# Kernel optimization log

Hardware: AMD Instinct MI355X
Metric: run time of the kernel (lower is better)

## Reference

```python
import jax, jax.numpy as jnp
import numpy as np

NUM_EMBEDDINGS = 2048
EMBEDDING_DIM = 512
INPUT_DIM = 256  # input_chan**2 = 16**2
COMMITMENT_COST = 0.25
BN_EPS = 1e-5


def setup_inputs() -> dict:
    key = jax.random.key(0)
    ks = jax.random.split(key, 8)
    B, N = 64, 1024
    inputs = jax.random.normal(ks[0], (B, N, INPUT_DIM), dtype=jnp.float32)
    # embedding init: uniform(-1/K, 1/K) as in the torch module
    emb_scale = 1.0 / NUM_EMBEDDINGS
    embedding = jax.random.uniform(ks[1], (NUM_EMBEDDINGS, EMBEDDING_DIM), dtype=jnp.float32,
                                   minval=-emb_scale, maxval=emb_scale)
    # Linear layers use torch convention W[out, in]
    W1 = jax.random.normal(ks[2], (EMBEDDING_DIM, INPUT_DIM), dtype=jnp.float32) / np.sqrt(INPUT_DIM)
    b1 = jnp.zeros((EMBEDDING_DIM,), dtype=jnp.float32)
    W2 = jax.random.normal(ks[3], (INPUT_DIM, EMBEDDING_DIM), dtype=jnp.float32) / np.sqrt(EMBEDDING_DIM)
    b2 = jnp.zeros((INPUT_DIM,), dtype=jnp.float32)
    # BatchNorm affine params initialized to 1/0 as in the module
    bn1_gamma = jnp.ones((INPUT_DIM,), dtype=jnp.float32)
    bn1_beta = jnp.zeros((INPUT_DIM,), dtype=jnp.float32)
    bn2_gamma = jnp.ones((EMBEDDING_DIM,), dtype=jnp.float32)
    bn2_beta = jnp.zeros((EMBEDDING_DIM,), dtype=jnp.float32)
    return {"inputs": inputs, "bn1_gamma": bn1_gamma, "bn1_beta": bn1_beta,
            "W1": W1, "b1": b1, "embedding": embedding,
            "bn2_gamma": bn2_gamma, "bn2_beta": bn2_beta, "W2": W2, "b2": b2}


def reference(inputs, bn1_gamma, bn1_beta, W1, b1, embedding, bn2_gamma, bn2_beta, W2, b2):
    sg = jax.lax.stop_gradient
    input_shape = inputs.shape
    flat = inputs.reshape(-1, INPUT_DIM)  # [T, D_in]
    # BatchNorm1d in eval mode (running_mean=0, running_var=1); Dropout is identity in eval.
    bn1_scale = 1.0 / jnp.sqrt(1.0 + BN_EPS)
    x = flat * (bn1_gamma * bn1_scale) + bn1_beta
    x = x @ W1.T + b1  # [T, E]
    # pairwise squared distances to codebook, argmin
    distances = (jnp.sum(x * x, axis=1, keepdims=True)
                 + jnp.sum(embedding * embedding, axis=1)
                 - 2.0 * x @ embedding.T)  # [T, K]
    encoding_indices = jnp.argmin(distances, axis=1)  # [T]
    # gather == one-hot @ embedding (same math, same gradient scatter-add)
    quantized = jnp.take(embedding, encoding_indices, axis=0)  # [T, E]
    bn2_scale = 1.0 / jnp.sqrt(1.0 + BN_EPS)
    quantized = quantized * (bn2_gamma * bn2_scale) + bn2_beta
    quantized = (quantized @ W2.T + b2).reshape(input_shape)
    e_latent_loss = jnp.mean((sg(quantized) - inputs) ** 2)
    q_latent_loss = jnp.mean((quantized - sg(inputs)) ** 2)
    loss = q_latent_loss + COMMITMENT_COST * e_latent_loss
    quantized_st = inputs + sg(quantized - inputs)  # straight-through
    T = flat.shape[0]
    usage = jnp.zeros((NUM_EMBEDDINGS,), dtype=jnp.float32).at[encoding_indices].add(1.0) / T
    return (loss, quantized_st, usage)
```

## Files before the change

kernel.cpp:

```cpp
#include <hip/hip_runtime.h>
#include <math.h>
#include <stdint.h>

#define TOK 65536
#define DIN 256
#define EDIM 512
#define KCB 2048
#define NTB 128

#define OFF_MP   0u
#define OFF_CP   524288u
#define OFF_Q    526336u
#define OFF_W2T  1050624u
#define OFF_U    1181696u
#define OFF_CQ   1182208u
#define OFF_BH   1182464u
#define TOT_F    1444608u

typedef short short8 __attribute__((ext_vector_type(8)));
typedef float f32x4 __attribute__((ext_vector_type(4)));

__device__ __forceinline__ unsigned short bf16rne(float x) {
    uint32_t u = __float_as_uint(x);
    u += 0x7fffu + ((u >> 16) & 1u);
    return (unsigned short)(u >> 16);
}
__device__ __forceinline__ void async_load16(const void* g, void* l) {
    __builtin_amdgcn_global_load_lds((const __attribute__((address_space(1))) void*)g,
                                     (__attribute__((address_space(3))) void*)l, 16, 0, 0);
}

__global__ void prep1_kernel(const float* __restrict__ W1, const float* __restrict__ W2,
                             const float* __restrict__ bn1_beta, const float* __restrict__ bn2_gamma,
                             const float* __restrict__ bn2_beta, const float* __restrict__ b2,
                             float* __restrict__ W2T, float* __restrict__ u, float* __restrict__ cQ,
                             float* __restrict__ out) {
    __shared__ float red[256];
    const int b = blockIdx.x, t = threadIdx.x;
    const int gid = b * 256 + t;
    if (gid == 0) out[0] = 0.0f;
    if (gid < KCB) out[1 + TOK * DIN + gid] = 0.0f;
    const float s = 1.0f / sqrtf(1.0f + 1e-5f);
    if (b < EDIM) {
        int e = b;
        W2T[e * DIN + t] = bn2_gamma[e] * s * W2[t * EDIM + e];
        float v = bn1_beta[t] * W1[e * DIN + t];
        red[t] = v; __syncthreads();
        for (int off = 128; off; off >>= 1) { if (t < off) red[t] += red[t + off]; __syncthreads(); }
        if (t == 0) u[e] = red[0];
    } else {
        int o = b - EDIM;
        float v = bn2_beta[t] * W2[o * EDIM + t] + bn2_beta[t + 256] * W2[o * EDIM + t + 256];
        red[t] = v; __syncthreads();
        for (int off = 128; off; off >>= 1) { if (t < off) red[t] += red[t + off]; __syncthreads(); }
        if (t == 0) cQ[o] = b2[o] + red[0];
    }
}

__global__ __launch_bounds__(512) void prep2_kernel(const float* __restrict__ E, const float* __restrict__ W1,
                                                    const float* __restrict__ W2T, const float* __restrict__ bn1_gamma,
                                                    const float* __restrict__ cQ, const float* __restrict__ b1,
                                                    const float* __restrict__ u,
                                                    float* __restrict__ Q, float* __restrict__ cp,
                                                    unsigned short* __restrict__ Bh) {
    __shared__ __align__(16) unsigned short hs[8][264];
    const int t = threadIdx.x;
    const int col = t & 255;
    const int half = __builtin_amdgcn_readfirstlane(t >> 8);
    const int k0 = blockIdx.x * 8;
    const float* __restrict__ Ek = E + ((size_t)k0 + (size_t)half * 4) * EDIM;

    float m[4] = {0, 0, 0, 0};
    float q[4] = {0, 0, 0, 0};
    for (int e0 = 0; e0 < EDIM; e0 += 8) {
        float w1v[8], w2v[8];
#pragma unroll
        for (int j = 0; j < 8; j++) {
            w1v[j] = W1[(e0 + j) * DIN + col];
            w2v[j] = W2T[(e0 + j) * DIN + col];
        }
#pragma unroll
        for (int r = 0; r < 4; r++) {
#pragma unroll
            for (int j = 0; j < 8; j++) {
                float ev = Ek[(size_t)r * EDIM + e0 + j];
                m[r] += ev * w1v[j];
                q[r] += ev * w2v[j];
            }
        }
    }
    const float s = 1.0f / sqrtf(1.0f + 1e-5f);
    const float gs = bn1_gamma[col] * s;
    const float cq = cQ[col];
#pragma unroll
    for (int r = 0; r < 4; r++) {
        Q[(size_t)(k0 + half * 4 + r) * DIN + col] = q[r] + cq;
        hs[half * 4 + r][col] = bf16rne(gs * m[r]);
    }

    {
        const int wv = t >> 6, l = t & 63;
        const float* __restrict__ Er = E + (size_t)(k0 + wv) * EDIM;
        float sa = 0.0f, sb = 0.0f;
#pragma unroll
        for (int i = 0; i < 8; i++) {
            int e = l + i * 64;
            float ev = Er[e];
            float be = b1[e] + u[e];
            sa += ev * be; sb += ev * ev;
        }
        float v = sa - 0.5f * sb;
#pragma unroll
        for (int off = 32; off; off >>= 1) v += __shfl_down(v, off, 64);
        if (l == 0) cp[k0 + wv] = v;
    }

    __syncthreads();

    if (t < 256) {
        const int rr = t & 7, qr = (t >> 3) & 3, kc = t >> 5;
        const int nt = k0 >> 4;
        const int l2 = (k0 & 8) + rr + (qr << 4);
        short8 vh = *(const short8*)&hs[rr][kc * 32 + qr * 8];
        *(short8*)&Bh[((size_t)kc * NTB + nt) * 512 + (size_t)l2 * 8] = vh;
    }
}

__global__ __launch_bounds__(256) void score_fused_kernel(const float* __restrict__ flat,
                                                          const unsigned short* __restrict__ Bh,
                                                          const float* __restrict__ cp,
                                                          const float* __restrict__ Q,
                                                          float* __restrict__ out) {
    __shared__ __align__(16) unsigned short Blds[2][32 * 512];
    __shared__ int ksel[128];
    const int t = threadIdx.x, lane = t & 63, w = t >> 6;
    const int m0 = blockIdx.x * 128;
    const int fr = lane & 15, qr = lane >> 4;

    short8 af[8][2];
#pragma unroll
    for (int kc = 0; kc < 8; kc++)
#pragma unroll
        for (int mt = 0; mt < 2; mt++) {
            int row = m0 + w * 32 + mt * 16 + fr;
            const float* p = flat + (size_t)row * DIN + kc * 32 + qr * 8;
            float4 a = *(const float4*)p;
            float4 b = *(const float4*)(p + 4);
            float f[8] = {a.x, a.y, a.z, a.w, b.x, b.y, b.z, b.w};
            unsigned short* hp = (unsigned short*)&af[kc][mt];
#pragma unroll
            for (int j = 0; j < 8; j++) hp[j] = bf16rne(f[j]);
        }

#pragma unroll
    for (int i = 0; i < 8; i++) {
        int tl = i * 4 + w;
        int kc = tl >> 2, nt = tl & 3;
        async_load16(Bh + ((size_t)kc * NTB + nt) * 512 + lane * 8,
                     &Blds[0][tl * 512 + lane * 8]);
    }
    __syncthreads();

    float bestv[2][4];
    int besti[2][4];
#pragma unroll
    for (int mt = 0; mt < 2; mt++)
#pragma unroll
        for (int r = 0; r < 4; r++) { bestv[mt][r] = -3.4e38f; besti[mt][r] = 0; }

    const f32x4 ZERO4 = {0.f, 0.f, 0.f, 0.f};

#pragma unroll 1
    for (int s = 0; s < 32; s++) {
        const int cur = s & 1;
        if (s < 31) {
            const int nxt = cur ^ 1;
#pragma unroll
            for (int i = 0; i < 8; i++) {
                int tl = i * 4 + w;
                int kc = tl >> 2, nt = tl & 3;
                async_load16(Bh + ((size_t)kc * NTB + (s + 1) * 4 + nt) * 512 + lane * 8,
                             &Blds[nxt][tl * 512 + lane * 8]);
            }
        }
        f32x4 acc[2][4];
        {
            short8 bf[4];
#pragma unroll
            for (int nt = 0; nt < 4; nt++)
                bf[nt] = *(const short8*)&Blds[cur][nt * 512 + lane * 8];
#pragma unroll
            for (int mt = 0; mt < 2; mt++)
#pragma unroll
                for (int nt = 0; nt < 4; nt++)
                    acc[mt][nt] = __builtin_amdgcn_mfma_f32_16x16x32_bf16(af[0][mt], bf[nt], ZERO4, 0, 0, 0);
        }
#pragma unroll
        for (int kc = 1; kc < 8; kc++) {
            short8 bf[4];
#pragma unroll
            for (int nt = 0; nt < 4; nt++)
                bf[nt] = *(const short8*)&Blds[cur][(kc * 4 + nt) * 512 + lane * 8];
#pragma unroll
            for (int mt = 0; mt < 2; mt++)
#pragma unroll
                for (int nt = 0; nt < 4; nt++)
                    acc[mt][nt] = __builtin_amdgcn_mfma_f32_16x16x32_bf16(af[kc][mt], bf[nt], acc[mt][nt], 0, 0, 0);
        }
        const int base = s * 64 + fr;
        float cpv[4];
        int cidx[4];
#pragma unroll
        for (int nt = 0; nt < 4; nt++) { cpv[nt] = cp[base + nt * 16]; cidx[nt] = base + nt * 16; }
#pragma unroll
        for (int mt = 0; mt < 2; mt++)
#pragma unroll
            for (int r = 0; r < 4; r++) {
                float v = acc[mt][0][r] + cpv[0];
                int ci = cidx[0];
#pragma unroll
                for (int nt = 1; nt < 4; nt++) {
                    float vi = acc[mt][nt][r] + cpv[nt];
                    if (vi > v) { v = vi; ci = cidx[nt]; }
                }
                if (v > bestv[mt][r]) { bestv[mt][r] = v; besti[mt][r] = ci; }
            }
        __syncthreads();
    }

#pragma unroll
    for (int mt = 0; mt < 2; mt++)
#pragma unroll
        for (int r = 0; r < 4; r++) {
            float bv = bestv[mt][r];
            int bc = besti[mt][r];
#pragma unroll
            for (int xm = 1; xm < 16; xm <<= 1) {
                float ov = __shfl_xor(bv, xm, 64);
                int oc = __shfl_xor(bc, xm, 64);
                if (ov > bv || (ov == bv && oc < bc)) { bv = ov; bc = oc; }
            }
            if (fr == 0) ksel[w * 32 + mt * 16 + qr * 4 + r] = bc;
        }
    __syncthreads();

    float lsum = 0.0f;
    for (int rr = 0; rr < 32; rr++) {
        int rl = w * 32 + rr;
        int row = m0 + rl;
        int k = ksel[rl];
        const float* qr_ = Q + (size_t)k * DIN;
        const float* xr = flat + (size_t)row * DIN;
        float* ob = out + 1 + (size_t)row * DIN;
#pragma unroll
        for (int cc = 0; cc < 4; cc++) {
            int j = lane + 64 * cc;
            float q = qr_[j];
            float d = q - xr[j];
            lsum += d * d;
            ob[j] = q;
        }
        if (lane == 0) atomicAdd(out + 1 + TOK * DIN + k, 1.0f / (float)TOK);
    }
#pragma unroll
    for (int off = 32; off; off >>= 1) lsum += __shfl_down(lsum, off, 64);
    if (lane == 0) atomicAdd(out, lsum * (1.25f / (float)((size_t)TOK * DIN)));
}

extern "C" void kernel_launch(void* const* d_in, const int* in_sizes, int n_in,
                              void* d_out, int out_size, void* d_ws, size_t ws_size,
                              hipStream_t stream) {
    const float* inputs = (const float*)d_in[0];
    const float* bn1_gamma = (const float*)d_in[1];
    const float* bn1_beta  = (const float*)d_in[2];
    const float* W1 = (const float*)d_in[3];
    const float* b1 = (const float*)d_in[4];
    const float* E  = (const float*)d_in[5];
    const float* bn2_gamma = (const float*)d_in[6];
    const float* bn2_beta  = (const float*)d_in[7];
    const float* W2 = (const float*)d_in[8];
    const float* b2 = (const float*)d_in[9];

    float* ws = (float*)d_ws;
    float* cp  = ws + OFF_CP;
    float* Q   = ws + OFF_Q;
    float* W2T = ws + OFF_W2T;
    float* u   = ws + OFF_U;
    float* cQ  = ws + OFF_CQ;
    unsigned short* Bh = (unsigned short*)(ws + OFF_BH);
    float* out = (float*)d_out;

    hipLaunchKernelGGL(prep1_kernel, dim3(768), dim3(256), 0, stream,
                       W1, W2, bn1_beta, bn2_gamma, bn2_beta, b2, W2T, u, cQ, out);
    hipLaunchKernelGGL(prep2_kernel, dim3(256), dim3(512), 0, stream,
                       E, W1, W2T, bn1_gamma, cQ, b1, u, Q, cp, Bh);
    hipLaunchKernelGGL(score_fused_kernel, dim3(512), dim3(256), 0, stream,
                       inputs, Bh, cp, Q, out);
}
```

Measured before the change: 264.1 us.

## Split score tile across 2x2 wave grid to halve LDS B-fragment reads

Each wave now covers 64 rows and half of the 64 codebook columns per stage (a 2x2 wave grid) instead of 32 rows and all 64 columns. Every B fragment read from LDS is reused across four row tiles, so each wave does half as many LDS loads per MFMA. Per-wave argmin partials are written to shared memory and merged across the two column halves, keeping the lowest-index tie-break. Holding four row tiles of A fragments in registers raises register pressure. Launch bounds now request 2 blocks per SM, which may cap registers and cause spills.

```diff
diff --git a/kernel.cpp b/kernel.cpp
--- a/kernel.cpp
+++ b/kernel.cpp
@@ -126,23 +126,25 @@
     }
 }
 
-__global__ __launch_bounds__(256) void score_fused_kernel(const float* __restrict__ flat,
-                                                          const unsigned short* __restrict__ Bh,
-                                                          const float* __restrict__ cp,
-                                                          const float* __restrict__ Q,
-                                                          float* __restrict__ out) {
+__global__ __launch_bounds__(256, 2) void score_fused_kernel(const float* __restrict__ flat,
+                                                             const unsigned short* __restrict__ Bh,
+                                                             const float* __restrict__ cp,
+                                                             const float* __restrict__ Q,
+                                                             float* __restrict__ out) {
     __shared__ __align__(16) unsigned short Blds[2][32 * 512];
-    __shared__ int ksel[128];
+    __shared__ float mv[2][128];
+    __shared__ int   mi[2][128];
     const int t = threadIdx.x, lane = t & 63, w = t >> 6;
+    const int wr = w >> 1, wc = w & 1;
     const int m0 = blockIdx.x * 128;
     const int fr = lane & 15, qr = lane >> 4;
 
-    short8 af[8][2];
+    short8 af[8][4];
 #pragma unroll
     for (int kc = 0; kc < 8; kc++)
 #pragma unroll
-        for (int mt = 0; mt < 2; mt++) {
-            int row = m0 + w * 32 + mt * 16 + fr;
+        for (int mt = 0; mt < 4; mt++) {
+            int row = m0 + wr * 64 + mt * 16 + fr;
             const float* p = flat + (size_t)row * DIN + kc * 32 + qr * 8;
             float4 a = *(const float4*)p;
             float4 b = *(const float4*)(p + 4);
@@ -161,10 +163,10 @@
     }
     __syncthreads();
 
-    float bestv[2][4];
-    int besti[2][4];
-#pragma unroll
-    for (int mt = 0; mt < 2; mt++)
+    float bestv[4][4];
+    int besti[4][4];
+#pragma unroll
+    for (int mt = 0; mt < 4; mt++)
 #pragma unroll
         for (int r = 0; r < 4; r++) { bestv[mt][r] = -3.4e38f; besti[mt][r] = 0; }
 
@@ -183,53 +185,44 @@
                              &Blds[nxt][tl * 512 + lane * 8]);
             }
         }
-        f32x4 acc[2][4];
+        f32x4 acc[4][2];
         {
-            short8 bf[4];
-#pragma unroll
-            for (int nt = 0; nt < 4; nt++)
-                bf[nt] = *(const short8*)&Blds[cur][nt * 512 + lane * 8];
-#pragma unroll
-            for (int mt = 0; mt < 2; mt++)
-#pragma unroll
-                for (int nt = 0; nt < 4; nt++)
-                    acc[mt][nt] = __builtin_amdgcn_mfma_f32_16x16x32_bf16(af[0][mt], bf[nt], ZERO4, 0, 0, 0);
+            short8 bf0 = *(const short8*)&Blds[cur][(0 * 4 + wc * 2 + 0) * 512 + lane * 8];
+            short8 bf1 = *(const short8*)&Blds[cur][(0 * 4 + wc * 2 + 1) * 512 + lane * 8];
+#pragma unroll
+            for (int mt = 0; mt < 4; mt++) {
+                acc[mt][0] = __builtin_amdgcn_mfma_f32_16x16x32_bf16(af[0][mt], bf0, ZERO4, 0, 0, 0);
+                acc[mt][1] = __builtin_amdgcn_mfma_f32_16x16x32_bf16(af[0][mt], bf1, ZERO4, 0, 0, 0);
+            }
         }
 #pragma unroll
         for (int kc = 1; kc < 8; kc++) {
-            short8 bf[4];
-#pragma unroll
-            for (int nt = 0; nt < 4; nt++)
-                bf[nt] = *(const short8*)&Blds[cur][(kc * 4 + nt) * 512 + lane * 8];
-#pragma unroll
-            for (int mt = 0; mt < 2; mt++)
-#pragma unroll
-                for (int nt = 0; nt < 4; nt++)
-                    acc[mt][nt] = __builtin_amdgcn_mfma_f32_16x16x32_bf16(af[kc][mt], bf[nt], acc[mt][nt], 0, 0, 0);
-        }
-        const int base = s * 64 + fr;
-        float cpv[4];
-        int cidx[4];
-#pragma unroll
-        for (int nt = 0; nt < 4; nt++) { cpv[nt] = cp[base + nt * 16]; cidx[nt] = base + nt * 16; }
-#pragma unroll
-        for (int mt = 0; mt < 2; mt++)
+            short8 bf0 = *(const short8*)&Blds[cur][(kc * 4 + wc * 2 + 0) * 512 + lane * 8];
+            short8 bf1 = *(const short8*)&Blds[cur][(kc * 4 + wc * 2 + 1) * 512 + lane * 8];
+#pragma unroll
+            for (int mt = 0; mt < 4; mt++) {
+                acc[mt][0] = __builtin_amdgcn_mfma_f32_16x16x32_bf16(af[kc][mt], bf0, acc[mt][0], 0, 0, 0);
+                acc[mt][1] = __builtin_amdgcn_mfma_f32_16x16x32_bf16(af[kc][mt], bf1, acc[mt][1], 0, 0, 0);
+            }
+        }
+        const int base = s * 64 + wc * 32 + fr;
+        const float cpv0 = cp[base];
+        const float cpv1 = cp[base + 16];
+#pragma unroll
+        for (int mt = 0; mt < 4; mt++)
 #pragma unroll
             for (int r = 0; r < 4; r++) {
-                float v = acc[mt][0][r] + cpv[0];
-                int ci = cidx[0];
-#pragma unroll
-                for (int nt = 1; nt < 4; nt++) {
-                    float vi = acc[mt][nt][r] + cpv[nt];
-                    if (vi > v) { v = vi; ci = cidx[nt]; }
-                }
+                float v0 = acc[mt][0][r] + cpv0;
+                float v1 = acc[mt][1][r] + cpv1;
+                float v = v0; int ci = base;
+                if (v1 > v0) { v = v1; ci = base + 16; }
                 if (v > bestv[mt][r]) { bestv[mt][r] = v; besti[mt][r] = ci; }
             }
         __syncthreads();
     }
 
 #pragma unroll
-    for (int mt = 0; mt < 2; mt++)
+    for (int mt = 0; mt < 4; mt++)
 #pragma unroll
         for (int r = 0; r < 4; r++) {
             float bv = bestv[mt][r];
@@ -240,7 +233,11 @@
                 int oc = __shfl_xor(bc, xm, 64);
                 if (ov > bv || (ov == bv && oc < bc)) { bv = ov; bc = oc; }
             }
-            if (fr == 0) ksel[w * 32 + mt * 16 + qr * 4 + r] = bc;
+            if (fr == 0) {
+                int rl = wr * 64 + mt * 16 + qr * 4 + r;
+                mv[wc][rl] = bv;
+                mi[wc][rl] = bc;
+            }
         }
     __syncthreads();
 
@@ -248,7 +245,9 @@
     for (int rr = 0; rr < 32; rr++) {
         int rl = w * 32 + rr;
         int row = m0 + rl;
-        int k = ksel[rl];
+        float v0 = mv[0][rl], v1 = mv[1][rl];
+        int c0 = mi[0][rl], c1 = mi[1][rl];
+        int k = (v1 > v0 || (v1 == v0 && c1 < c0)) ? c1 : c0;
         const float* qr_ = Q + (size_t)k * DIN;
         const float* xr = flat + (size_t)row * DIN;
         float* ob = out + 1 + (size_t)row * DIN;
```

Measured after the change: 274.7 us. 4.0% more time.
